# Kernel tuning notes

Hardware: AMD Instinct MI355X
Metric: run time of the kernel (lower is better)

## Reference

```python
import jax, jax.numpy as jnp
import numpy as np

B, L1, L2, H = 16, 1024, 1024, 768

def setup_inputs() -> dict:
    key = jax.random.key(0)
    k1, k2, k3, k4, k5, k6 = jax.random.split(key, 6)
    x1 = jax.random.normal(k1, (B, L1, H), dtype=jnp.float32)
    x2 = jax.random.normal(k2, (B, L2, H), dtype=jnp.float32)
    # True = padded position (masked out), matching torch masked_fill_ semantics
    x1_mask = jax.random.randint(k3, (B, L1), 0, 2) == 1
    x2_mask = jax.random.randint(k4, (B, L2), 0, 2) == 1
    # shared nn.Linear(H, H) used for both x and y projections
    W = jax.random.normal(k5, (H, H), dtype=jnp.float32) / np.sqrt(H)
    b = jax.random.normal(k6, (H,), dtype=jnp.float32) * 0.01
    return {"x1": x1, "x2": x2, "x1_mask": x1_mask, "x2_mask": x2_mask, "W": W, "b": b}

def reference(x1, x2, x1_mask, x2_mask, W, b):
    # SeqAttnMatch('relu_FC', normalize='sumY') with z = y = x2
    x_proj = jax.nn.relu(jnp.einsum('bid,hd->bih', x1, W) + b)   # [B,L1,H]
    y_proj = jax.nn.relu(jnp.einsum('bjd,hd->bjh', x2, W) + b)   # [B,L2,H]
    scores = jnp.einsum('bih,bjh->bij', x_proj, y_proj)          # [B,L1,L2]
    scores = jnp.where(x2_mask[:, None, :], -jnp.inf, scores)
    alpha = jax.nn.softmax(scores, axis=-1)                      # sum over len2
    att = jnp.einsum('bij,bjd->bid', alpha, x2)                  # [B,L1,H]
    # inter_att_concat = 'concat_dot_diff'
    return jnp.concatenate([x1, att, x1 * att, x1 - att], axis=2)  # [B,L1,4H]
```

## Files before the change

### kernel.cpp

```cpp
#include <hip/hip_runtime.h>


#define B_  16
#define L_  1024
#define H_  768
#define M1_ (B_ * L_)
#define MT_ (2 * M1_)

#define XB_  24576
#define WB_  576
#define TB_  3072

using f32x4  = __attribute__((ext_vector_type(4))) float;
using bf16x8 = __attribute__((ext_vector_type(8))) __bf16;
using u16x8  = __attribute__((ext_vector_type(8))) unsigned short;
using u16x4  = __attribute__((ext_vector_type(4))) unsigned short;

__device__ inline unsigned short f2b(float f) {
  unsigned u = __builtin_bit_cast(unsigned, f);
  u += 0x7FFFu + ((u >> 16) & 1u);
  return (unsigned short)(u >> 16);
}
__device__ inline float b2f(unsigned short u) {
  return __builtin_bit_cast(float, ((unsigned)u) << 16);
}

__device__ inline void gld16(const void* g, void* l) {
  __builtin_amdgcn_global_load_lds(
      (__attribute__((address_space(1))) void*)g,
      (__attribute__((address_space(3))) void*)l, 16, 0, 0);
}

__device__ inline bf16x8 ld_frag_sw(const unsigned short* lds, int row, int quad) {
  const int sl = quad ^ ((row >> 1) & 3);
  u16x8 v = *(const u16x8*)(lds + row * 32 + sl * 8);
  return __builtin_bit_cast(bf16x8, v);
}

#define MFMA(a, b, c) __builtin_amdgcn_mfma_f32_16x16x32_bf16((a), (b), (c), 0, 0, 0)

template<int CH>
__device__ __forceinline__ void stageH(const unsigned short* __restrict__ src,
                                       unsigned short* ldsbase,
                                       int wv, int lq, int lsw,
                                       size_t row0, int k0) {
#pragma unroll
  for (int g = 0; g < CH; ++g) {
    const int rowl = wv * (CH * 16) + g * 16;
    gld16(src + (row0 + rowl + lq) * (size_t)H_ + k0 + lsw * 8,
          ldsbase + rowl * 32);
  }
}

template<int MI>
__device__ __forceinline__ void gemm3_loop(
    const unsigned short* __restrict__ Agh, const unsigned short* __restrict__ Agl,
    const unsigned short* __restrict__ Bgh, const unsigned short* __restrict__ Bgl,
    size_t arow0, size_t brow0,
    unsigned short* SA, unsigned short* SB, f32x4 (&acc)[MI][4])
{
  constexpr int CA  = MI / 4;
  constexpr int HBA = (MI * 32) * 32;
  constexpr int HBB = 256 * 32;

  const int tid  = threadIdx.x;
  const int lane = tid & 63, wv = tid >> 6;
  const int wr = wv >> 2, wc = wv & 3;
  const int quad = lane >> 4, lx = lane & 15;
  const int lq  = lane >> 2;
  const int lsw = (lane & 3) ^ ((lane >> 3) & 3);

  stageH<CA>(Agh, SA,       wv, lq, lsw, arow0, 0);
  stageH<2 >(Bgh, SB,       wv, lq, lsw, brow0, 0);
  stageH<2 >(Bgl, SB + HBB, wv, lq, lsw, brow0, 0);
  stageH<CA>(Agl, SA + HBA, wv, lq, lsw, arow0, 0);
  asm volatile("s_waitcnt vmcnt(%0)" :: "i"(CA + 2) : "memory");
  __builtin_amdgcn_s_barrier();

  int c = 0;
  for (int t = 0; t < H_ / 32; ++t) {
    unsigned short* sAh = SA + c * (2 * HBA);
    unsigned short* sAl = sAh + HBA;
    unsigned short* sBh = SB + c * (2 * HBB);
    unsigned short* sBl = sBh + HBB;
    unsigned short* dA  = SA + (c ^ 1) * (2 * HBA);
    unsigned short* dB  = SB + (c ^ 1) * (2 * HBB);
    const int  k1   = t * 32 + 32;
    const bool more = (t < H_ / 32 - 1);

    bf16x8 fah[MI], fbh[4];
#pragma unroll
    for (int i = 0; i < MI; ++i)
      fah[i] = ld_frag_sw(sAh, wr * (MI * 16) + i * 16 + lx, quad);
#pragma unroll
    for (int j = 0; j < 4; ++j)
      fbh[j] = ld_frag_sw(sBh, wc * 64 + j * 16 + lx, quad);
    if (more) {
      stageH<CA>(Agh, dA, wv, lq, lsw, arow0, k1);
      stageH<2 >(Bgh, dB, wv, lq, lsw, brow0, k1);
    }
    __builtin_amdgcn_s_barrier();
    __builtin_amdgcn_s_setprio(1);
#pragma unroll
    for (int i = 0; i < MI; ++i)
#pragma unroll
      for (int j = 0; j < 4; ++j) acc[i][j] = MFMA(fah[i], fbh[j], acc[i][j]);
    __builtin_amdgcn_s_setprio(0);
    if (more) asm volatile("s_waitcnt vmcnt(%0)" :: "i"(2 * CA + 2) : "memory");
    else      asm volatile("s_waitcnt vmcnt(%0)" :: "i"(CA)         : "memory");
    __builtin_amdgcn_s_barrier();

    bf16x8 fbl[4];
#pragma unroll
    for (int j = 0; j < 4; ++j)
      fbl[j] = ld_frag_sw(sBl, wc * 64 + j * 16 + lx, quad);
    if (more) stageH<2>(Bgl, dB + HBB, wv, lq, lsw, brow0, k1);
    __builtin_amdgcn_s_barrier();
    __builtin_amdgcn_s_setprio(1);
#pragma unroll
    for (int i = 0; i < MI; ++i)
#pragma unroll
      for (int j = 0; j < 4; ++j) acc[i][j] = MFMA(fah[i], fbl[j], acc[i][j]);
    __builtin_amdgcn_s_setprio(0);
    if (more) asm volatile("s_waitcnt vmcnt(%0)" :: "i"(CA + 4) : "memory");
    else      asm volatile("s_waitcnt vmcnt(0)" ::: "memory");
    __builtin_amdgcn_s_barrier();

    bf16x8 fal[MI];
#pragma unroll
    for (int i = 0; i < MI; ++i)
      fal[i] = ld_frag_sw(sAl, wr * (MI * 16) + i * 16 + lx, quad);
    if (more) stageH<CA>(Agl, dA + HBA, wv, lq, lsw, arow0, k1);
    __builtin_amdgcn_s_barrier();
    __builtin_amdgcn_s_setprio(1);
#pragma unroll
    for (int i = 0; i < MI; ++i)
#pragma unroll
      for (int j = 0; j < 4; ++j) acc[i][j] = MFMA(fal[i], fbh[j], acc[i][j]);
    __builtin_amdgcn_s_setprio(0);
    if (more) asm volatile("s_waitcnt vmcnt(%0)" :: "i"(CA + 2) : "memory");
    __builtin_amdgcn_s_barrier();

    c ^= 1;
  }
}

__global__ __launch_bounds__(256) void k_split(
    const float* __restrict__ x1, const float* __restrict__ x2,
    const float* __restrict__ W,
    unsigned short* __restrict__ Xh, unsigned short* __restrict__ Xl,
    unsigned short* __restrict__ Wh, unsigned short* __restrict__ Wl,
    unsigned short* __restrict__ x2T)
{
  __shared__ unsigned short tile[64][72];
  const int tid = threadIdx.x;
  const int bx  = blockIdx.x;

  if (bx < XB_) {
    const size_t idx = (size_t)bx * 256 + tid;
    const int row = (int)(idx / 192);
    const int col = ((int)(idx % 192)) * 4;
    const float* src = (row < M1_) ? (x1 + (size_t)row * H_ + col)
                                   : (x2 + (size_t)(row - M1_) * H_ + col);
    f32x4 v = *(const f32x4*)src;
    u16x4 h, l;
#pragma unroll
    for (int q = 0; q < 4; ++q) { h[q] = f2b(v[q]); l[q] = f2b(v[q] - b2f(h[q])); }
    *(u16x4*)(Xh + idx * 4) = h;
    *(u16x4*)(Xl + idx * 4) = l;
  } else if (bx < XB_ + WB_) {
    const int idx = (bx - XB_) * 256 + tid;
    f32x4 v = *(const f32x4*)(W + (size_t)idx * 4);
    u16x4 h, l;
#pragma unroll
    for (int q = 0; q < 4; ++q) { h[q] = f2b(v[q]); l[q] = f2b(v[q] - b2f(h[q])); }
    *(u16x4*)(Wh + (size_t)idx * 4) = h;
    *(u16x4*)(Wl + (size_t)idx * 4) = l;
  } else {
    const int t  = bx - (XB_ + WB_);
    const int b  = t / 192;
    const int r  = t % 192;
    const int j0 = (r / 12) * 64;
    const int d0 = (r % 12) * 64;
#pragma unroll
    for (int p = 0; p < 4; ++p) {
      const int idx = tid + p * 256;
      const int jr  = idx >> 4;
      const int dc  = (idx & 15) * 4;
      f32x4 v = *(const f32x4*)(x2 + ((size_t)(b * L_ + j0 + jr)) * H_ + d0 + dc);
#pragma unroll
      for (int q = 0; q < 4; ++q) tile[jr][dc + q] = f2b(v[q]);
    }
    __syncthreads();
#pragma unroll
    for (int p = 0; p < 2; ++p) {
      const int idx = tid + p * 256;
      const int dr  = idx >> 3;
      const int jc  = (idx & 7) * 8;
      u16x8 o;
#pragma unroll
      for (int q = 0; q < 8; ++q) o[q] = tile[jc + q][dr];
      *(u16x8*)(x2T + ((size_t)(b * H_) + d0 + dr) * L_ + j0 + jc) = o;
    }
  }
}

__global__ __launch_bounds__(512, 2) void k_proj(
    const unsigned short* __restrict__ Xh, const unsigned short* __restrict__ Xl,
    const unsigned short* __restrict__ Wh, const unsigned short* __restrict__ Wl,
    const float* __restrict__ bias,
    unsigned short* __restrict__ Ph, unsigned short* __restrict__ Pl)
{
  __shared__ unsigned short SA[2 * 2 * 128 * 32];
  __shared__ unsigned short SB[2 * 2 * 256 * 32];

  const int tid  = threadIdx.x;
  const int lane = tid & 63, wv = tid >> 6;
  const int wr = wv >> 2, wc = wv & 3;
  const int quad = lane >> 4, lx = lane & 15;

  const int lin = blockIdx.x;
  const int s   = (lin & 7) * 96 + (lin >> 3);
  const int n0  = (s % 3) * 256;
  const int m0  = (s / 3) * 128;

  f32x4 acc[4][4] = {};
  gemm3_loop<4>(Xh, Xl, Wh, Wl, (size_t)m0, (size_t)n0, SA, SB, acc);

#pragma unroll
  for (int j = 0; j < 4; ++j) {
    const int h = n0 + wc * 64 + j * 16 + lx;
    const float bv = bias[h];
#pragma unroll
    for (int i = 0; i < 4; ++i) {
      const int mrow = m0 + wr * 64 + i * 16 + quad * 4;
#pragma unroll
      for (int r = 0; r < 4; ++r) {
        float v = acc[i][j][r] + bv;
        v = v > 0.f ? v : 0.f;
        const unsigned short hh = f2b(v);
        const unsigned short ll = f2b(v - b2f(hh));
        const size_t off = (size_t)(mrow + r) * H_ + h;
        Ph[off] = hh;
        Pl[off] = ll;
      }
    }
  }
}

__global__ __launch_bounds__(512, 2) void k_scores(
    const unsigned short* __restrict__ Ph, const unsigned short* __restrict__ Pl,
    const int* __restrict__ x2_mask, float* __restrict__ scores)
{
  __shared__ unsigned short SA[2 * 2 * 256 * 32];
  __shared__ unsigned short SB[2 * 2 * 256 * 32];

  const int tid  = threadIdx.x;
  const int lane = tid & 63, wv = tid >> 6;
  const int wr = wv >> 2, wc = wv & 3;
  const int quad = lane >> 4, lx = lane & 15;

  const int lin = blockIdx.x;
  const int s   = (lin & 7) * 32 + (lin >> 3);
  const int j0  = (s & 3) * 256;
  const int i0  = ((s >> 2) & 3) * 256;
  const int b   = s >> 4;

  f32x4 acc[8][4] = {};
  gemm3_loop<8>(Ph, Pl, Ph, Pl,
                (size_t)(b * L_ + i0), (size_t)(M1_ + b * L_ + j0), SA, SB, acc);

#pragma unroll
  for (int j = 0; j < 4; ++j) {
    const int jj = j0 + wc * 64 + j * 16 + lx;
    const int mv = x2_mask[b * L_ + jj];
#pragma unroll
    for (int i = 0; i < 8; ++i) {
      const int ib = i0 + wr * 128 + i * 16 + quad * 4;
#pragma unroll
      for (int r = 0; r < 4; ++r) {
        const float v = mv ? -1e30f : acc[i][j][r];
        scores[((size_t)(b * L_) + ib + r) * L_ + jj] = v;
      }
    }
  }
}

__global__ __launch_bounds__(256) void k_softmax(
    const float* __restrict__ scores, unsigned short* __restrict__ alphab)
{
  const size_t row = blockIdx.x;
  const float* p = scores + row * L_;
  const int tid = threadIdx.x;

  f32x4 v = *(const f32x4*)(p + tid * 4);
  float m = fmaxf(fmaxf(v[0], v[1]), fmaxf(v[2], v[3]));
#pragma unroll
  for (int off = 32; off > 0; off >>= 1) m = fmaxf(m, __shfl_down(m, off));

  __shared__ float rmax[4];
  __shared__ float rsum[4];
  const int wid = tid >> 6, lane = tid & 63;
  if (lane == 0) rmax[wid] = m;
  __syncthreads();
  m = fmaxf(fmaxf(rmax[0], rmax[1]), fmaxf(rmax[2], rmax[3]));

  f32x4 e;
#pragma unroll
  for (int q = 0; q < 4; ++q) e[q] = __expf(v[q] - m);
  float s = e[0] + e[1] + e[2] + e[3];
#pragma unroll
  for (int off = 32; off > 0; off >>= 1) s += __shfl_down(s, off);
  if (lane == 0) rsum[wid] = s;
  __syncthreads();
  s = rsum[0] + rsum[1] + rsum[2] + rsum[3];

  const float inv = 1.0f / s;
  u16x4 o;
#pragma unroll
  for (int q = 0; q < 4; ++q) o[q] = f2b(e[q] * inv);
  *(u16x4*)(alphab + row * L_ + tid * 4) = o;
}

__global__ __launch_bounds__(256) void k_att(
    const unsigned short* __restrict__ alphab, const unsigned short* __restrict__ x2T,
    float* __restrict__ att)
{
  __shared__ unsigned short Aa[128 * 32];
  __shared__ unsigned short Bt[128 * 32];

  const int tid  = threadIdx.x;
  const int lane = tid & 63, wv = tid >> 6;
  const int wr = wv >> 1, wc = wv & 1;
  const int quad = lane >> 4, lx = lane & 15;
  const int lr = lane >> 2, ls = lane & 3;
  const int lsw = ls ^ ((lr >> 1) & 3);

  const int lin = blockIdx.x;
  const int s   = (lin & 7) * 96 + (lin >> 3);
  const int d0  = (s % 6) * 128;
  const int i0  = ((s / 6) & 7) * 128;
  const int b   = s / 48;

  f32x4 acc[4][4] = {};

  for (int j0 = 0; j0 < L_; j0 += 32) {
    __syncthreads();
#pragma unroll
    for (int g = 0; g < 2; ++g) {
      const int rowl = wv * 32 + g * 16;
      const int row  = rowl + lr;
      const size_t ga = (size_t)(b * L_ + i0 + row) * L_ + j0 + lsw * 8;
      const size_t gb = ((size_t)(b * H_) + d0 + row) * L_ + j0 + lsw * 8;
      gld16(alphab + ga, &Aa[rowl * 32]);
      gld16(x2T + gb, &Bt[rowl * 32]);
    }
    __syncthreads();

    bf16x8 fa[4], fb[4];
#pragma unroll
    for (int t = 0; t < 4; ++t) {
      fa[t] = ld_frag_sw(Aa, wr * 64 + t * 16 + lx, quad);
      fb[t] = ld_frag_sw(Bt, wc * 64 + t * 16 + lx, quad);
    }
#pragma unroll
    for (int i = 0; i < 4; ++i)
#pragma unroll
      for (int j = 0; j < 4; ++j)
        acc[i][j] = MFMA(fa[i], fb[j], acc[i][j]);
  }

#pragma unroll
  for (int j = 0; j < 4; ++j) {
    const int dd = d0 + wc * 64 + j * 16 + lx;
#pragma unroll
    for (int i = 0; i < 4; ++i) {
      const int ib = i0 + wr * 64 + i * 16 + quad * 4;
#pragma unroll
      for (int r = 0; r < 4; ++r)
        att[((size_t)(b * L_) + ib + r) * H_ + dd] = acc[i][j][r];
    }
  }
}

__global__ __launch_bounds__(256) void k_concat(
    const float* __restrict__ x1, const float* __restrict__ att,
    float* __restrict__ out)
{
  const int gid = blockIdx.x * 256 + threadIdx.x;
  const int row = gid / 192;
  const int c   = (gid % 192) * 4;

  f32x4 xv = *(const f32x4*)(x1  + (size_t)row * H_ + c);
  f32x4 av = *(const f32x4*)(att + (size_t)row * H_ + c);
  f32x4 mv, sv;
#pragma unroll
  for (int q = 0; q < 4; ++q) { mv[q] = xv[q] * av[q]; sv[q] = xv[q] - av[q]; }

  float* ob = out + (size_t)row * (4 * H_) + c;
  *(f32x4*)(ob)          = xv;
  *(f32x4*)(ob + H_)     = av;
  *(f32x4*)(ob + 2 * H_) = mv;
  *(f32x4*)(ob + 3 * H_) = sv;
}

extern "C" void kernel_launch(void* const* d_in, const int* in_sizes, int n_in,
                              void* d_out, int out_size, void* d_ws, size_t ws_size,
                              hipStream_t stream) {
  const float* x1      = (const float*)d_in[0];
  const float* x2      = (const float*)d_in[1];
  const int*   x2_mask = (const int*)d_in[3];
  const float* W       = (const float*)d_in[4];
  const float* bias    = (const float*)d_in[5];
  float* out = (float*)d_out;

  char* o8 = (char*)d_out;
  unsigned short* Ph     = (unsigned short*)o8;
  unsigned short* Pl     = (unsigned short*)(o8 + 50331648);
  float*          scores = (float*)(o8 + 100663296);
  unsigned short* Xh     = (unsigned short*)(o8 + 100663296);
  unsigned short* Wh     = (unsigned short*)(o8 + 167772160);
  unsigned short* Wl     = (unsigned short*)(o8 + 168951808);
  unsigned short* x2T    = (unsigned short*)(o8 + 170131456);
  unsigned short* alphab = (unsigned short*)o8;
  unsigned short* Xl     = (unsigned short*)d_ws;
  float*          att    = (float*)d_ws;

  k_split  <<<dim3(XB_ + WB_ + TB_), 256, 0, stream>>>(x1, x2, W, Xh, Xl, Wh, Wl, x2T);
  k_proj   <<<dim3(768),   512, 0, stream>>>(Xh, Xl, Wh, Wl, bias, Ph, Pl);
  k_scores <<<dim3(256),   512, 0, stream>>>(Ph, Pl, x2_mask, scores);
  k_softmax<<<dim3(16384), 256, 0, stream>>>(scores, alphab);
  k_att    <<<dim3(768),   256, 0, stream>>>(alphab, x2T, att);
  k_concat <<<dim3(12288), 256, 0, stream>>>(x1, att, out);
}
```

Measured before the change: 588.5 us.

## Fuse attention-weighted sum with concat epilogue and triple-buffer att loop

Adds a k_attcat kernel that computes att and writes the four concat outputs straight from registers, dropping the separate att buffer and the k_concat pass. It runs only when the workspace is large enough, and alphab and x2T move into the workspace so the output buffer is not overwritten while it is being written. The att loop now uses a three-stage async LDS pipeline with one barrier per step instead of two syncthreads around each load. Several barriers and waitcnts are also dropped from the projection GEMM main loop. The risks are LDS race hazards from the fewer barriers and uncoalesced scattered stores in the fused epilogue.

After: 586.9 us. About the same (-0.3%).

```diff
diff --git a/kernel.cpp b/kernel.cpp
--- a/kernel.cpp
+++ b/kernel.cpp
@@ -99,15 +99,14 @@
       stageH<CA>(Agh, dA, wv, lq, lsw, arow0, k1);
       stageH<2 >(Bgh, dB, wv, lq, lsw, brow0, k1);
     }
-    __builtin_amdgcn_s_barrier();
     __builtin_amdgcn_s_setprio(1);
 #pragma unroll
     for (int i = 0; i < MI; ++i)
 #pragma unroll
       for (int j = 0; j < 4; ++j) acc[i][j] = MFMA(fah[i], fbh[j], acc[i][j]);
     __builtin_amdgcn_s_setprio(0);
-    if (more) asm volatile("s_waitcnt vmcnt(%0)" :: "i"(2 * CA + 2) : "memory");
-    else      asm volatile("s_waitcnt vmcnt(%0)" :: "i"(CA)         : "memory");
+    if (more) asm volatile("s_waitcnt vmcnt(%0)" :: "i"(CA + 2) : "memory");
+    else      asm volatile("s_waitcnt vmcnt(0)" ::: "memory");
     __builtin_amdgcn_s_barrier();
 
     bf16x8 fbl[4];
@@ -115,32 +114,28 @@
     for (int j = 0; j < 4; ++j)
       fbl[j] = ld_frag_sw(sBl, wc * 64 + j * 16 + lx, quad);
     if (more) stageH<2>(Bgl, dB + HBB, wv, lq, lsw, brow0, k1);
-    __builtin_amdgcn_s_barrier();
     __builtin_amdgcn_s_setprio(1);
 #pragma unroll
     for (int i = 0; i < MI; ++i)
 #pragma unroll
       for (int j = 0; j < 4; ++j) acc[i][j] = MFMA(fah[i], fbl[j], acc[i][j]);
     __builtin_amdgcn_s_setprio(0);
-    if (more) asm volatile("s_waitcnt vmcnt(%0)" :: "i"(CA + 4) : "memory");
-    else      asm volatile("s_waitcnt vmcnt(0)" ::: "memory");
-    __builtin_amdgcn_s_barrier();
 
     bf16x8 fal[MI];
 #pragma unroll
     for (int i = 0; i < MI; ++i)
       fal[i] = ld_frag_sw(sAl, wr * (MI * 16) + i * 16 + lx, quad);
     if (more) stageH<CA>(Agl, dA + HBA, wv, lq, lsw, arow0, k1);
-    __builtin_amdgcn_s_barrier();
     __builtin_amdgcn_s_setprio(1);
 #pragma unroll
     for (int i = 0; i < MI; ++i)
 #pragma unroll
       for (int j = 0; j < 4; ++j) acc[i][j] = MFMA(fal[i], fbh[j], acc[i][j]);
     __builtin_amdgcn_s_setprio(0);
-    if (more) asm volatile("s_waitcnt vmcnt(%0)" :: "i"(CA + 2) : "memory");
-    __builtin_amdgcn_s_barrier();
-
+    if (more) {
+      asm volatile("s_waitcnt vmcnt(%0)" :: "i"(CA + 2) : "memory");
+      __builtin_amdgcn_s_barrier();
+    }
     c ^= 1;
   }
 }
@@ -322,19 +317,81 @@
   *(u16x4*)(alphab + row * L_ + tid * 4) = o;
 }
 
-__global__ __launch_bounds__(256) void k_att(
+__device__ __forceinline__ void att_loop(
     const unsigned short* __restrict__ alphab, const unsigned short* __restrict__ x2T,
-    float* __restrict__ att)
-{
-  __shared__ unsigned short Aa[128 * 32];
-  __shared__ unsigned short Bt[128 * 32];
+    int b, int i0, int d0, unsigned short* AS, f32x4 (&acc)[4][4])
+{
+  constexpr int HB = 128 * 32;
 
   const int tid  = threadIdx.x;
   const int lane = tid & 63, wv = tid >> 6;
   const int wr = wv >> 1, wc = wv & 1;
   const int quad = lane >> 4, lx = lane & 15;
-  const int lr = lane >> 2, ls = lane & 3;
-  const int lsw = ls ^ ((lr >> 1) & 3);
+  const int lq  = lane >> 2;
+  const int lsw = (lane & 3) ^ ((lane >> 3) & 3);
+
+  unsigned short* a0 = AS;            unsigned short* b0 = AS + 3 * HB;
+  unsigned short* a1 = AS + HB;       unsigned short* b1 = AS + 4 * HB;
+  unsigned short* a2 = AS + 2 * HB;   unsigned short* b2 = AS + 5 * HB;
+
+  const size_t abase = (size_t)(b * L_ + i0) * L_;
+  const size_t bbase = ((size_t)(b * H_) + d0) * L_;
+
+#define ATT_STAGE(pa, pb, jt)                                                  \
+  {                                                                            \
+    const int j0s = (jt) * 32;                                                 \
+    _Pragma("unroll")                                                          \
+    for (int g = 0; g < 2; ++g) {                                              \
+      const int rowl = wv * 32 + g * 16;                                       \
+      gld16(alphab + abase + (size_t)(rowl + lq) * L_ + j0s + lsw * 8,         \
+            (pa) + rowl * 32);                                                 \
+    }                                                                          \
+    _Pragma("unroll")                                                          \
+    for (int g = 0; g < 2; ++g) {                                              \
+      const int rowl = wv * 32 + g * 16;                                       \
+      gld16(x2T + bbase + (size_t)(rowl + lq) * L_ + j0s + lsw * 8,            \
+            (pb) + rowl * 32);                                                 \
+    }                                                                          \
+  }
+
+  ATT_STAGE(a0, b0, 0)
+  ATT_STAGE(a1, b1, 1)
+  asm volatile("s_waitcnt vmcnt(4)" ::: "memory");
+  __builtin_amdgcn_s_barrier();
+
+  for (int t = 0; t < 32; ++t) {
+    bf16x8 fa[4], fb[4];
+#pragma unroll
+    for (int i = 0; i < 4; ++i) fa[i] = ld_frag_sw(a0, wr * 64 + i * 16 + lx, quad);
+#pragma unroll
+    for (int j = 0; j < 4; ++j) fb[j] = ld_frag_sw(b0, wc * 64 + j * 16 + lx, quad);
+    if (t + 2 < 32) ATT_STAGE(a2, b2, t + 2)
+    __builtin_amdgcn_s_setprio(1);
+#pragma unroll
+    for (int i = 0; i < 4; ++i)
+#pragma unroll
+      for (int j = 0; j < 4; ++j) acc[i][j] = MFMA(fa[i], fb[j], acc[i][j]);
+    __builtin_amdgcn_s_setprio(0);
+    if (t + 2 < 32)      asm volatile("s_waitcnt vmcnt(4)" ::: "memory");
+    else if (t == 30)    asm volatile("s_waitcnt vmcnt(0)" ::: "memory");
+    if (t < 31) __builtin_amdgcn_s_barrier();
+    unsigned short* ta = a0; a0 = a1; a1 = a2; a2 = ta;
+    unsigned short* tb = b0; b0 = b1; b1 = b2; b2 = tb;
+  }
+#undef ATT_STAGE
+}
+
+__global__ __launch_bounds__(256) void k_att(
+    const unsigned short* __restrict__ alphab, const unsigned short* __restrict__ x2T,
+    float* __restrict__ att)
+{
+  __shared__ unsigned short AS[6 * 128 * 32];
+
+  const int tid  = threadIdx.x;
+  const int lane = tid & 63, wv = tid >> 6;
+  const int wr = wv >> 1, wc = wv & 1;
+  const int quad = lane >> 4, lx = lane & 15;
+  (void)wv;
 
   const int lin = blockIdx.x;
   const int s   = (lin & 7) * 96 + (lin >> 3);
@@ -343,32 +400,7 @@
   const int b   = s / 48;
 
   f32x4 acc[4][4] = {};
-
-  for (int j0 = 0; j0 < L_; j0 += 32) {
-    __syncthreads();
-#pragma unroll
-    for (int g = 0; g < 2; ++g) {
-      const int rowl = wv * 32 + g * 16;
-      const int row  = rowl + lr;
-      const size_t ga = (size_t)(b * L_ + i0 + row) * L_ + j0 + lsw * 8;
-      const size_t gb = ((size_t)(b * H_) + d0 + row) * L_ + j0 + lsw * 8;
-      gld16(alphab + ga, &Aa[rowl * 32]);
-      gld16(x2T + gb, &Bt[rowl * 32]);
-    }
-    __syncthreads();
-
-    bf16x8 fa[4], fb[4];
-#pragma unroll
-    for (int t = 0; t < 4; ++t) {
-      fa[t] = ld_frag_sw(Aa, wr * 64 + t * 16 + lx, quad);
-      fb[t] = ld_frag_sw(Bt, wc * 64 + t * 16 + lx, quad);
-    }
-#pragma unroll
-    for (int i = 0; i < 4; ++i)
-#pragma unroll
-      for (int j = 0; j < 4; ++j)
-        acc[i][j] = MFMA(fa[i], fb[j], acc[i][j]);
-  }
+  att_loop(alphab, x2T, b, i0, d0, AS, acc);
 
 #pragma unroll
   for (int j = 0; j < 4; ++j) {
@@ -379,6 +411,48 @@
 #pragma unroll
       for (int r = 0; r < 4; ++r)
         att[((size_t)(b * L_) + ib + r) * H_ + dd] = acc[i][j][r];
+    }
+  }
+}
+
+__global__ __launch_bounds__(256) void k_attcat(
+    const unsigned short* __restrict__ alphab, const unsigned short* __restrict__ x2T,
+    const float* __restrict__ x1, float* __restrict__ out)
+{
+  __shared__ unsigned short AS[6 * 128 * 32];
+
+  const int tid  = threadIdx.x;
+  const int lane = tid & 63, wv = tid >> 6;
+  const int wr = wv >> 1, wc = wv & 1;
+  const int quad = lane >> 4, lx = lane & 15;
+  (void)wv;
+
+  const int lin = blockIdx.x;
+  const int s   = (lin & 7) * 96 + (lin >> 3);
+  const int d0  = (s % 6) * 128;
+  const int i0  = ((s / 6) & 7) * 128;
+  const int b   = s / 48;
+
+  f32x4 acc[4][4] = {};
+  att_loop(alphab, x2T, b, i0, d0, AS, acc);
+
+#pragma unroll
+  for (int j = 0; j < 4; ++j) {
+    const int dd = d0 + wc * 64 + j * 16 + lx;
+#pragma unroll
+    for (int i = 0; i < 4; ++i) {
+      const int ib = i0 + wr * 64 + i * 16 + quad * 4;
+#pragma unroll
+      for (int r = 0; r < 4; ++r) {
+        const size_t row = (size_t)(b * L_) + ib + r;
+        const float xv = x1[row * H_ + dd];
+        const float av = acc[i][j][r];
+        float* ob = out + row * (4 * H_) + dd;
+        ob[0]      = xv;
+        ob[H_]     = av;
+        ob[2 * H_] = xv * av;
+        ob[3 * H_] = xv - av;
+      }
     }
   }
 }
@@ -415,21 +489,30 @@
   float* out = (float*)d_out;
 
   char* o8 = (char*)d_out;
+  char* w8 = (char*)d_ws;
   unsigned short* Ph     = (unsigned short*)o8;
   unsigned short* Pl     = (unsigned short*)(o8 + 50331648);
   float*          scores = (float*)(o8 + 100663296);
   unsigned short* Xh     = (unsigned short*)(o8 + 100663296);
   unsigned short* Wh     = (unsigned short*)(o8 + 167772160);
   unsigned short* Wl     = (unsigned short*)(o8 + 168951808);
-  unsigned short* x2T    = (unsigned short*)(o8 + 170131456);
-  unsigned short* alphab = (unsigned short*)o8;
   unsigned short* Xl     = (unsigned short*)d_ws;
+
+  const bool fused = (ws_size >= (size_t)75497472);
+  unsigned short* x2T    = fused ? (unsigned short*)(w8 + 50331648)
+                                 : (unsigned short*)(o8 + 170131456);
+  unsigned short* alphab = fused ? (unsigned short*)w8
+                                 : (unsigned short*)o8;
   float*          att    = (float*)d_ws;
 
   k_split  <<<dim3(XB_ + WB_ + TB_), 256, 0, stream>>>(x1, x2, W, Xh, Xl, Wh, Wl, x2T);
   k_proj   <<<dim3(768),   512, 0, stream>>>(Xh, Xl, Wh, Wl, bias, Ph, Pl);
   k_scores <<<dim3(256),   512, 0, stream>>>(Ph, Pl, x2_mask, scores);
   k_softmax<<<dim3(16384), 256, 0, stream>>>(scores, alphab);
-  k_att    <<<dim3(768),   256, 0, stream>>>(alphab, x2T, att);
-  k_concat <<<dim3(12288), 256, 0, stream>>>(x1, att, out);
-}
+  if (fused) {
+    k_attcat<<<dim3(768),  256, 0, stream>>>(alphab, x2T, x1, out);
+  } else {
+    k_att   <<<dim3(768),  256, 0, stream>>>(alphab, x2T, att);
+    k_concat<<<dim3(12288), 256, 0, stream>>>(x1, att, out);
+  }
+}
```
